# Kernel tuning notes

Measured on AMD Instinct MI355X. Metric: run time of the kernel, lower is better.

The kernel has to match this reference:

```python
import jax, jax.numpy as jnp
import numpy as np

KV_CACHE_SIZE = 8192
DIM = 128
BBPM_MEM_SIZE = 131072
B, T = 32, 8192
N_TOKENS = B * T  # 262144


def setup_inputs() -> dict:
    key = jax.random.key(0)
    k1, k2, k3 = jax.random.split(key, 3)
    keys = jax.random.randint(k1, (B, T), 0, 1000000, dtype=jnp.int64)
    values = jax.random.normal(k2, (B, T, DIM), dtype=jnp.float32)
    positions = jnp.arange(N_TOKENS, dtype=jnp.int64).reshape(B, T)
    query_keys = jax.random.randint(k3, (B, T), 0, 1000000, dtype=jnp.int64)
    query_positions = jax.random.randint(
        jax.random.fold_in(key, 7), (B, T), 0, N_TOKENS, dtype=jnp.int64)
    bbpm_mem = jnp.zeros((BBPM_MEM_SIZE, DIM), dtype=jnp.float32)
    return {"keys": keys, "values": values, "positions": positions,
            "query_keys": query_keys, "query_positions": query_positions,
            "bbpm_mem": bbpm_mem}


def reference(keys, values, positions, query_keys, query_positions, bbpm_mem):
    # --- write_to_cache ---
    keys_f = keys.reshape(-1)                  # [n]
    vals_f = values.reshape(-1, DIM)           # [n, d]
    pos_f = positions.reshape(-1)              # [n]
    n = keys_f.shape[0]

    # BBPM write: hashed additive associative memory (scatter-add).
    mem = bbpm_mem.at[keys_f % BBPM_MEM_SIZE].add(vals_f)

    # Ring-cache write: cache_ptr starts at 0 and K | n, so the sequential
    # overwrite loop leaves exactly the last K tokens: slot idx holds token
    # i = n - K + idx. (Original writes values into both k_cache and v_cache;
    # only v_cache is read.)
    K = KV_CACHE_SIZE
    v_cache = vals_f[n - K:]                   # [K, d]
    cache_positions = pos_f[n - K:]            # [K], unique

    # --- retrieve ---
    qkeys = query_keys.reshape(-1)             # [Q]
    qpos = query_positions.reshape(-1)         # [Q]

    # Position -> cache-slot map (positions are unique, so scatter-set is
    # equivalent to taking the first matching slot).
    pos_table = jnp.full((N_TOKENS,), -1, dtype=jnp.int32)
    pos_table = pos_table.at[cache_positions].set(
        jnp.arange(K, dtype=jnp.int32))
    idx = pos_table[qpos]                      # [Q]
    hit = idx >= 0

    cache_vals = v_cache[jnp.maximum(idx, 0)]          # [Q, d]
    bbpm_vals = mem[qkeys % BBPM_MEM_SIZE]             # [Q, d]
    out = jnp.where(hit[:, None], cache_vals, bbpm_vals)  # [Q, d]
    return out
```

## Files before the change

### kernel.cpp

```cpp
#include <hip/hip_runtime.h>


typedef float f32x4 __attribute__((ext_vector_type(4)));
typedef int   i32x4 __attribute__((ext_vector_type(4)));

constexpr int DIM    = 128;
constexpr int MEM    = 131072;
constexpr int KCACHE = 8192;
constexpr int CAP    = 8;

__device__ __forceinline__ f32x4 ldrow(const float* __restrict__ p, int q) {
    return *reinterpret_cast<const f32x4*>(p + q * 4);
}
__device__ __forceinline__ f32x4 nt_ldrow(const float* __restrict__ p, int q) {
    return __builtin_nontemporal_load(reinterpret_cast<const f32x4*>(p) + q);
}
__device__ __forceinline__ void nt_strow(float* __restrict__ p, int q, f32x4 v) {
    __builtin_nontemporal_store(v, reinterpret_cast<f32x4*>(p) + q);
}

__global__ void fill_kernel(const int* __restrict__ keys,
                            int* __restrict__ cnt, int* __restrict__ bucket,
                            int* __restrict__ ovf_cnt, int* __restrict__ ovf, int n) {
    int i = blockIdx.x * 256 + threadIdx.x;
    if (i >= n) return;
    int slot = ((unsigned)keys[i]) & (MEM - 1);
    int pos = atomicAdd(&cnt[slot], 1);
    if (pos < CAP) bucket[slot * CAP + pos] = i;
    else { int k = atomicAdd(ovf_cnt, 1); ovf[k] = i; }
}

__global__ void build_pos_kernel(const int* __restrict__ positions,
                                 int* __restrict__ pos_table, int n, int K) {
    int j = blockIdx.x * 256 + threadIdx.x;
    if (j >= K) return;
    int p = positions[n - K + j];
    if (p >= 0 && p < n) pos_table[p] = j;
}

__global__ void qfill_kernel(const int* __restrict__ qkeys,
                             const int* __restrict__ qpos,
                             const int* __restrict__ pos_table,
                             int* __restrict__ qflag, int n) {
    int r = blockIdx.x * 256 + threadIdx.x;
    if (r >= n) return;
    int qp = qpos[r];
    int idx = (qp >= 0 && qp < n) ? pos_table[qp] : -1;
    if (idx < 0) qflag[((unsigned)qkeys[r]) & (MEM - 1)] = 1;
}

__global__ void reduce_kernel(const float* __restrict__ vals,
                              const float* __restrict__ bbpm,
                              const int* __restrict__ cnt,
                              const int* __restrict__ qflag,
                              const int* __restrict__ bucket,
                              float* __restrict__ acc,
                              const f32x4* __restrict__ vals4, int nv4) {
    {
        int chunk = (nv4 + gridDim.x - 1) / gridDim.x;
        int beg = blockIdx.x * chunk;
        int end = beg + chunk; if (end > nv4) end = nv4;
        float s = 0.f;
        for (int t = beg + (int)threadIdx.x; t < end; t += 256) {
            f32x4 v = vals4[t];
            s += v.x + v.y + v.z + v.w;
        }
        asm volatile("" :: "v"(s));
    }

    int g = threadIdx.x >> 5;
    int q = threadIdx.x & 31;
    int s0 = blockIdx.x * 16 + g;
    int s1 = s0 + 8;

    int f0 = qflag[s0], f1 = qflag[s1];
    if ((f0 | f1) == 0) return;

    int c0 = f0 ? cnt[s0] : 0; if (c0 > CAP) c0 = CAP;
    int c1 = f1 ? cnt[s1] : 0; if (c1 > CAP) c1 = CAP;
    i32x4 b0 = *reinterpret_cast<const i32x4*>(bucket + s0 * CAP);
    i32x4 b1 = *reinterpret_cast<const i32x4*>(bucket + s1 * CAP);

    int r00 = c0 > 0 ? b0.x : 0, r01 = c0 > 1 ? b0.y : 0;
    int r10 = c1 > 0 ? b1.x : 0, r11 = c1 > 1 ? b1.y : 0;
    float m00 = c0 > 0 ? 1.f : 0.f, m01 = c0 > 1 ? 1.f : 0.f;
    float m10 = c1 > 0 ? 1.f : 0.f, m11 = c1 > 1 ? 1.f : 0.f;

    const float* bb0 = bbpm + (f0 ? (size_t)s0 * DIM : 0);
    const float* bb1 = bbpm + (f1 ? (size_t)s1 * DIM : 0);
    f32x4 A0  = nt_ldrow(bb0, q);
    f32x4 A1  = nt_ldrow(bb1, q);
    f32x4 V00 = ldrow(vals + (size_t)r00 * DIM, q);
    f32x4 V01 = ldrow(vals + (size_t)r01 * DIM, q);
    f32x4 V10 = ldrow(vals + (size_t)r10 * DIM, q);
    f32x4 V11 = ldrow(vals + (size_t)r11 * DIM, q);

    f32x4 a0 = A0 + m00 * V00 + m01 * V01;
    f32x4 a1 = A1 + m10 * V10 + m11 * V11;

    if (c0 > 2) {
        a0 += ldrow(vals + (size_t)b0.z * DIM, q);
        if (c0 > 3) {
            a0 += ldrow(vals + (size_t)b0.w * DIM, q);
            for (int j = 4; j < c0; ++j)
                a0 += ldrow(vals + (size_t)bucket[s0 * CAP + j] * DIM, q);
        }
    }
    if (c1 > 2) {
        a1 += ldrow(vals + (size_t)b1.z * DIM, q);
        if (c1 > 3) {
            a1 += ldrow(vals + (size_t)b1.w * DIM, q);
            for (int j = 4; j < c1; ++j)
                a1 += ldrow(vals + (size_t)bucket[s1 * CAP + j] * DIM, q);
        }
    }

    if (f0) *reinterpret_cast<f32x4*>(acc + (size_t)s0 * DIM + q * 4) = a0;
    if (f1) *reinterpret_cast<f32x4*>(acc + (size_t)s1 * DIM + q * 4) = a1;
}

__global__ void overflow_kernel(const float* __restrict__ vals,
                                const int* __restrict__ keys,
                                const int* __restrict__ ovf_cnt,
                                const int* __restrict__ ovf,
                                float* __restrict__ acc) {
    int total = *ovf_cnt;
    int tid = blockIdx.x * 256 + threadIdx.x, stride = gridDim.x * 256;
    for (int w = tid; w < total * 32; w += stride) {
        int e = w >> 5, q = w & 31;
        int i = ovf[e];
        int slot = ((unsigned)keys[i]) & (MEM - 1);
        f32x4 v = ldrow(vals + (size_t)i * DIM, q);
        float* dst = acc + (size_t)slot * DIM + q * 4;
        atomicAdd(dst + 0, v.x);
        atomicAdd(dst + 1, v.y);
        atomicAdd(dst + 2, v.z);
        atomicAdd(dst + 3, v.w);
    }
}

__global__ void gather_kernel(const float* __restrict__ vals,
                              const float* __restrict__ acc,
                              const int* __restrict__ qkeys,
                              const int* __restrict__ qpos,
                              const int* __restrict__ pos_table,
                              float* __restrict__ out, int n, int base) {
    int g = threadIdx.x >> 5;
    int q = threadIdx.x & 31;
    int r0 = blockIdx.x * 32 + g;
    int r1 = r0 + 8, r2 = r0 + 16, r3 = r0 + 24;

    bool k0 = r0 < n, k1 = r1 < n, k2 = r2 < n, k3 = r3 < n;
    int qp0 = k0 ? qpos[r0] : -1, qp1 = k1 ? qpos[r1] : -1;
    int qp2 = k2 ? qpos[r2] : -1, qp3 = k3 ? qpos[r3] : -1;
    int qk0 = k0 ? qkeys[r0] : 0, qk1 = k1 ? qkeys[r1] : 0;
    int qk2 = k2 ? qkeys[r2] : 0, qk3 = k3 ? qkeys[r3] : 0;

    int i0 = (qp0 >= 0 && qp0 < n) ? pos_table[qp0] : -1;
    int i1 = (qp1 >= 0 && qp1 < n) ? pos_table[qp1] : -1;
    int i2 = (qp2 >= 0 && qp2 < n) ? pos_table[qp2] : -1;
    int i3 = (qp3 >= 0 && qp3 < n) ? pos_table[qp3] : -1;

    const float* s0 = (i0 >= 0) ? vals + (size_t)(base + i0) * DIM
                                : acc + (size_t)(((unsigned)qk0) & (MEM - 1)) * DIM;
    const float* s1 = (i1 >= 0) ? vals + (size_t)(base + i1) * DIM
                                : acc + (size_t)(((unsigned)qk1) & (MEM - 1)) * DIM;
    const float* s2 = (i2 >= 0) ? vals + (size_t)(base + i2) * DIM
                                : acc + (size_t)(((unsigned)qk2) & (MEM - 1)) * DIM;
    const float* s3 = (i3 >= 0) ? vals + (size_t)(base + i3) * DIM
                                : acc + (size_t)(((unsigned)qk3) & (MEM - 1)) * DIM;

    f32x4 v0 = ldrow(s0, q);
    f32x4 v1 = ldrow(s1, q);
    f32x4 v2 = ldrow(s2, q);
    f32x4 v3 = ldrow(s3, q);

    if (k0) nt_strow(out + (size_t)r0 * DIM, q, v0);
    if (k1) nt_strow(out + (size_t)r1 * DIM, q, v1);
    if (k2) nt_strow(out + (size_t)r2 * DIM, q, v2);
    if (k3) nt_strow(out + (size_t)r3 * DIM, q, v3);
}

extern "C" void kernel_launch(void* const* d_in, const int* in_sizes, int n_in,
                              void* d_out, int out_size, void* d_ws, size_t ws_size,
                              hipStream_t stream) {
    const int*   keys      = (const int*)d_in[0];
    const float* vals      = (const float*)d_in[1];
    const int*   positions = (const int*)d_in[2];
    const int*   qkeys     = (const int*)d_in[3];
    const int*   qpos      = (const int*)d_in[4];
    const float* bbpm      = (const float*)d_in[5];
    float* out = (float*)d_out;

    const int n = in_sizes[0];

    char* ws = (char*)d_ws;
    int*   cnt       = (int*)ws;
    int*   qflag     = cnt + MEM;
    int*   ctrs      = qflag + MEM;
    int*   pos_table = ctrs + 64;
    int*   bucket    = pos_table + n;
    int*   ovf       = bucket + MEM * CAP;
    float* acc       = (float*)(ovf + n);

    hipMemsetAsync(cnt, 0, (size_t)(2 * MEM + 64) * 4, stream);
    hipMemsetAsync(pos_table, 0xFF, (size_t)n * 4, stream);

    fill_kernel<<<(n + 255) / 256, 256, 0, stream>>>(keys, cnt, bucket, &ctrs[0], ovf, n);
    build_pos_kernel<<<(KCACHE + 255) / 256, 256, 0, stream>>>(positions, pos_table, n, KCACHE);
    qfill_kernel<<<(n + 255) / 256, 256, 0, stream>>>(qkeys, qpos, pos_table, qflag, n);
    reduce_kernel<<<MEM / 16, 256, 0, stream>>>(vals, bbpm, cnt, qflag, bucket, acc,
                                                (const f32x4*)vals, n * (DIM / 4));
    overflow_kernel<<<64, 256, 0, stream>>>(vals, keys, &ctrs[0], ovf, acc);
    gather_kernel<<<(n + 31) / 32, 256, 0, stream>>>(vals, acc, qkeys, qpos, pos_table,
                                                     out, n, n - KCACHE);
}
```

Before: 129.8 us.

## Fuse key bucketing and query flagging into one front kernel with value prefetch

Merges the key-bucketing fill kernel and the query-flag kernel into one launch, which runs after build_pos. The streaming read of the values array, used to warm the cache, moves out of reduce_kernel into this new front kernel. reduce_kernel gets launch bounds and loads counts and buckets before its early-exit test, so that latency overlaps. This removes one launch and a dependency point, and the cache-warming pass now overlaps the atomic-heavy bucketing instead of the reduce phase.

```diff
diff --git a/kernel.cpp b/kernel.cpp
--- a/kernel.cpp
+++ b/kernel.cpp
@@ -17,17 +17,6 @@
 }
 __device__ __forceinline__ void nt_strow(float* __restrict__ p, int q, f32x4 v) {
     __builtin_nontemporal_store(v, reinterpret_cast<f32x4*>(p) + q);
-}
-
-__global__ void fill_kernel(const int* __restrict__ keys,
-                            int* __restrict__ cnt, int* __restrict__ bucket,
-                            int* __restrict__ ovf_cnt, int* __restrict__ ovf, int n) {
-    int i = blockIdx.x * 256 + threadIdx.x;
-    if (i >= n) return;
-    int slot = ((unsigned)keys[i]) & (MEM - 1);
-    int pos = atomicAdd(&cnt[slot], 1);
-    if (pos < CAP) bucket[slot * CAP + pos] = i;
-    else { int k = atomicAdd(ovf_cnt, 1); ovf[k] = i; }
 }
 
 __global__ void build_pos_kernel(const int* __restrict__ positions,
@@ -38,48 +27,59 @@
     if (p >= 0 && p < n) pos_table[p] = j;
 }
 
-__global__ void qfill_kernel(const int* __restrict__ qkeys,
+__global__ void front_kernel(const int* __restrict__ keys,
+                             int* __restrict__ cnt, int* __restrict__ bucket,
+                             int* __restrict__ ovf_cnt, int* __restrict__ ovf,
+                             const int* __restrict__ qkeys,
                              const int* __restrict__ qpos,
                              const int* __restrict__ pos_table,
-                             int* __restrict__ qflag, int n) {
-    int r = blockIdx.x * 256 + threadIdx.x;
-    if (r >= n) return;
-    int qp = qpos[r];
-    int idx = (qp >= 0 && qp < n) ? pos_table[qp] : -1;
-    if (idx < 0) qflag[((unsigned)qkeys[r]) & (MEM - 1)] = 1;
-}
-
-__global__ void reduce_kernel(const float* __restrict__ vals,
-                              const float* __restrict__ bbpm,
-                              const int* __restrict__ cnt,
-                              const int* __restrict__ qflag,
-                              const int* __restrict__ bucket,
-                              float* __restrict__ acc,
-                              const f32x4* __restrict__ vals4, int nv4) {
-    {
-        int chunk = (nv4 + gridDim.x - 1) / gridDim.x;
-        int beg = blockIdx.x * chunk;
-        int end = beg + chunk; if (end > nv4) end = nv4;
-        float s = 0.f;
-        for (int t = beg + (int)threadIdx.x; t < end; t += 256) {
-            f32x4 v = vals4[t];
-            s += v.x + v.y + v.z + v.w;
-        }
-        asm volatile("" :: "v"(s));
-    }
-
+                             int* __restrict__ qflag,
+                             const f32x4* __restrict__ vals4,
+                             int n, int nv4) {
+    int tid = blockIdx.x * 256 + threadIdx.x;
+
+    if (tid < n) {
+        int slot = ((unsigned)keys[tid]) & (MEM - 1);
+        int pos = atomicAdd(&cnt[slot], 1);
+        if (pos < CAP) bucket[slot * CAP + pos] = tid;
+        else { int k = atomicAdd(ovf_cnt, 1); ovf[k] = tid; }
+    }
+    if (tid < n) {
+        int qp = qpos[tid];
+        int idx = (qp >= 0 && qp < n) ? pos_table[qp] : -1;
+        if (idx < 0) qflag[((unsigned)qkeys[tid]) & (MEM - 1)] = 1;
+    }
+    int chunk = (nv4 + gridDim.x - 1) / gridDim.x;
+    int beg = blockIdx.x * chunk;
+    int end = beg + chunk; if (end > nv4) end = nv4;
+    float s = 0.f;
+    for (int t = beg + (int)threadIdx.x; t < end; t += 256) {
+        f32x4 v = vals4[t];
+        s += v.x + v.y + v.z + v.w;
+    }
+    asm volatile("" :: "v"(s));
+}
+
+__global__ void __launch_bounds__(256, 8)
+reduce_kernel(const float* __restrict__ vals,
+              const float* __restrict__ bbpm,
+              const int* __restrict__ cnt,
+              const int* __restrict__ qflag,
+              const int* __restrict__ bucket,
+              float* __restrict__ acc) {
     int g = threadIdx.x >> 5;
     int q = threadIdx.x & 31;
     int s0 = blockIdx.x * 16 + g;
     int s1 = s0 + 8;
 
     int f0 = qflag[s0], f1 = qflag[s1];
-    if ((f0 | f1) == 0) return;
-
-    int c0 = f0 ? cnt[s0] : 0; if (c0 > CAP) c0 = CAP;
-    int c1 = f1 ? cnt[s1] : 0; if (c1 > CAP) c1 = CAP;
+    int n0 = cnt[s0],   n1 = cnt[s1];
     i32x4 b0 = *reinterpret_cast<const i32x4*>(bucket + s0 * CAP);
     i32x4 b1 = *reinterpret_cast<const i32x4*>(bucket + s1 * CAP);
+    if ((f0 | f1) == 0) return;
+
+    int c0 = f0 ? (n0 > CAP ? CAP : n0) : 0;
+    int c1 = f1 ? (n1 > CAP ? CAP : n1) : 0;
 
     int r00 = c0 > 0 ? b0.x : 0, r01 = c0 > 1 ? b0.y : 0;
     int r10 = c1 > 0 ? b1.x : 0, r11 = c1 > 1 ? b1.y : 0;
@@ -206,11 +206,13 @@
     hipMemsetAsync(cnt, 0, (size_t)(2 * MEM + 64) * 4, stream);
     hipMemsetAsync(pos_table, 0xFF, (size_t)n * 4, stream);
 
-    fill_kernel<<<(n + 255) / 256, 256, 0, stream>>>(keys, cnt, bucket, &ctrs[0], ovf, n);
-    build_pos_kernel<<<(KCACHE + 255) / 256, 256, 0, stream>>>(positions, pos_table, n, KCACHE);
-    qfill_kernel<<<(n + 255) / 256, 256, 0, stream>>>(qkeys, qpos, pos_table, qflag, n);
-    reduce_kernel<<<MEM / 16, 256, 0, stream>>>(vals, bbpm, cnt, qflag, bucket, acc,
-                                                (const f32x4*)vals, n * (DIM / 4));
+    build_pos_kernel<<<(KCACHE + 255) / 256, 256, 0, stream>>>(positions, pos_table,
+                                                               n, KCACHE);
+    front_kernel<<<(n + 255) / 256, 256, 0, stream>>>(
+        keys, cnt, bucket, &ctrs[0], ovf,
+        qkeys, qpos, pos_table, qflag,
+        (const f32x4*)vals, n, n * (DIM / 4));
+    reduce_kernel<<<MEM / 16, 256, 0, stream>>>(vals, bbpm, cnt, qflag, bucket, acc);
     overflow_kernel<<<64, 256, 0, stream>>>(vals, keys, &ctrs[0], ovf, acc);
     gather_kernel<<<(n + 31) / 32, 256, 0, stream>>>(vals, acc, qkeys, qpos, pos_table,
                                                      out, n, n - KCACHE);
```

Measured after the change: 128.3 us. About the same (-1.2%).
